# Kernel tuning notes

Measured on AMD Instinct MI355X. Metric: run time of the kernel, lower is better.

Reference implementation:

```python
import jax, jax.numpy as jnp
import numpy as np

N = 100000   # nodes
E = 1600000  # edges (avg degree 16)
D = 32       # feature dim

def setup_inputs() -> dict:
    key = jax.random.key(0)
    k1, k2, k3, k4 = jax.random.split(key, 4)
    feat = jax.random.normal(k1, (N, D), dtype=jnp.float32)
    e_feat = jax.random.normal(k2, (E, 1), dtype=jnp.float32)
    src = jax.random.randint(k3, (E,), 0, N)
    dst = jax.random.randint(k4, (E,), 0, N)
    return {"feat": feat, "e_feat": e_feat, "src": src, "dst": dst}

def reference(feat, e_feat, src, dst):
    n = feat.shape[0]
    ones = jnp.ones(src.shape[0], dtype=feat.dtype)
    # degrees computed on the full graph (before self-loop removal), as in DGL code
    out_deg = jax.ops.segment_sum(ones, src, num_segments=n)
    in_deg = jax.ops.segment_sum(ones, dst, num_segments=n)
    src_norm = jnp.power(jnp.clip(out_deg, 1.0, None), -0.5)[:, None]  # [N,1]
    dst_norm = jnp.power(jnp.clip(in_deg, 1.0, None), -0.5)[:, None]   # [N,1]
    # remove_self_loop: mask out self-loop edges in the aggregation only
    mask = (src != dst).astype(feat.dtype)[:, None]                    # [E,1]
    # u_mul_e: gather normalized src features, multiply by edge weight
    msg = (feat * src_norm)[src] * (e_feat * mask)                     # [E,D]
    agg = jax.ops.segment_sum(msg, dst, num_segments=n)                # [N,D]
    out = feat - agg * dst_norm
    return jnp.sum(jnp.abs(out), axis=1)                               # [N]
```

## Files before the change

kernel.cpp:

```cpp
#include <hip/hip_runtime.h>

#define D 32
#define RANGE 128
#define RMAX 800
#define JC 512
#define SCAN_CHUNK 4096
#define CAP 2560

__global__ void count_kernel(const int* __restrict__ src, const int* __restrict__ dst,
                             int* __restrict__ cnt, int E, int R, int chunk) {
    __shared__ int cd[RMAX];
    __shared__ int cs[RMAX];
    int j = blockIdx.x;
    for (int i = threadIdx.x; i < R; i += blockDim.x) { cd[i] = 0; cs[i] = 0; }
    __syncthreads();
    int e0 = j * chunk, e1 = min(E, e0 + chunk);
    for (int e = e0 + threadIdx.x; e < e1; e += blockDim.x) {
        atomicAdd(&cd[dst[e] >> 7], 1);
        atomicAdd(&cs[src[e] >> 7], 1);
    }
    __syncthreads();
    for (int i = threadIdx.x; i < R; i += blockDim.x) {
        cnt[(size_t)i * JC + j]       = cd[i];
        cnt[(size_t)(R + i) * JC + j] = cs[i];
    }
}

__global__ void scan_part(const int* __restrict__ deg, int* __restrict__ offsets,
                          int* __restrict__ blockSums, int n) {
    __shared__ int lds[256];
    int t = threadIdx.x;
    int base = blockIdx.x * SCAN_CHUNK + t * 16;
    int v[16];
    int tsum = 0;
#pragma unroll
    for (int i = 0; i < 16; i++) {
        int idx = base + i;
        int x = (idx < n) ? deg[idx] : 0;
        v[i] = tsum;
        tsum += x;
    }
    lds[t] = tsum;
    __syncthreads();
    for (int off = 1; off < 256; off <<= 1) {
        int val = (t >= off) ? lds[t - off] : 0;
        __syncthreads();
        lds[t] += val;
        __syncthreads();
    }
    int texcl = (t == 0) ? 0 : lds[t - 1];
    if (t == 255) blockSums[blockIdx.x] = lds[255];
#pragma unroll
    for (int i = 0; i < 16; i++) {
        int idx = base + i;
        if (idx < n) offsets[idx] = texcl + v[i];
    }
}

__global__ void scan_top(int* __restrict__ blockSums, int nb) {
    __shared__ int lds[256];
    int t = threadIdx.x;
    lds[t] = (t < nb) ? blockSums[t] : 0;
    __syncthreads();
    for (int off = 1; off < 256; off <<= 1) {
        int val = (t >= off) ? lds[t - off] : 0;
        __syncthreads();
        lds[t] += val;
        __syncthreads();
    }
    if (t < nb) blockSums[t] = (t == 0) ? 0 : lds[t - 1];
}

__global__ void scan_add(int* __restrict__ offsets, const int* __restrict__ blockSums, int n) {
    int i = blockIdx.x * blockDim.x + threadIdx.x;
    if (i < n) offsets[i] += blockSums[i / SCAN_CHUNK];
}

__global__ void reorder_kernel(const int* __restrict__ src, const int* __restrict__ dst,
                               const float* __restrict__ ef, const int* __restrict__ offs,
                               unsigned int* __restrict__ recsS_m, uint2* __restrict__ recs,
                               int E, int R, int chunk) {
    __shared__ int curD[RMAX];
    __shared__ int curS[RMAX];
    int j = blockIdx.x;
    for (int i = threadIdx.x; i < R; i += blockDim.x) {
        curD[i] = offs[(size_t)i * JC + j];
        curS[i] = offs[(size_t)(R + i) * JC + j];
    }
    __syncthreads();
    int e0 = j * chunk, e1 = min(E, e0 + chunk);
    for (int e = e0 + threadIdx.x; e < e1; e += blockDim.x) {
        int s = src[e], d = dst[e];
        int ps = atomicAdd(&curS[s >> 7], 1);
        recsS_m[ps] = (unsigned)s;
        float w = (s == d) ? 0.0f : ef[e];
        int pd = atomicAdd(&curD[d >> 7], 1);
        recs[pd] = make_uint2((unsigned)s | ((unsigned)(d & (RANGE - 1)) << 17),
                              __float_as_uint(w));
    }
}

__device__ __forceinline__ unsigned short f2bf(float x) {
    unsigned u = __float_as_uint(x);
    u += 0x7FFFu + ((u >> 16) & 1u);
    return (unsigned short)(u >> 16);
}

__global__ void srcnorm_convert(const unsigned int* __restrict__ recsS_m,
                                const int* __restrict__ offs, const float* __restrict__ feat,
                                unsigned short* __restrict__ featb, int E, int n, int R) {
    __shared__ int cnt[RANGE];
    int r = blockIdx.x;
    int base = r * RANGE;
    int lim = min(n - base, RANGE);
    for (int i = threadIdx.x; i < RANGE; i += blockDim.x) cnt[i] = 0;
    __syncthreads();
    int start = offs[(size_t)(R + r) * JC];
    int end = (r + 1 < R) ? offs[(size_t)(R + r + 1) * JC] : 2 * E;
    for (int i = start + threadIdx.x; i < end; i += blockDim.x)
        atomicAdd(&cnt[recsS_m[i] - base], 1);
    __syncthreads();
    int total4 = lim * 8;
    for (int i = threadIdx.x; i < total4; i += blockDim.x) {
        int row = i >> 3;
        float sn = rsqrtf((float)max(cnt[row], 1));
        float4 f = ((const float4*)(feat + (size_t)(base + row) * D))[i & 7];
        ushort4 u;
        u.x = f2bf(f.x * sn); u.y = f2bf(f.y * sn);
        u.z = f2bf(f.z * sn); u.w = f2bf(f.w * sn);
        ((ushort4*)(featb + (size_t)(base + row) * D))[i & 7] = u;
    }
}

__global__ __launch_bounds__(512) void gather_kernel(
        const float* __restrict__ feat, const unsigned short* __restrict__ featb,
        const uint2* __restrict__ recs, const int* __restrict__ offs,
        float* __restrict__ out, int E, int n, int R) {
    __shared__ uint2 srec[CAP];
    __shared__ int indeg[RANGE];
    __shared__ int pre[RANGE + 1];
    __shared__ int cur[RANGE];
    int r = blockIdx.x;
    int base = r * RANGE;
    int lim = min(n - base, RANGE);
    int start = offs[(size_t)r * JC];
    int end = (r + 1 < R) ? offs[(size_t)(r + 1) * JC] : E;
    int capEnd = min(end, start + CAP);
    for (int i = threadIdx.x; i < RANGE; i += blockDim.x) indeg[i] = 0;
    __syncthreads();
    for (int i = start + threadIdx.x; i < capEnd; i += blockDim.x)
        atomicAdd(&indeg[(recs[i].x >> 17) & 0x1FFu], 1);
    __syncthreads();
    if (threadIdx.x < RANGE) pre[threadIdx.x + 1] = indeg[threadIdx.x];
    if (threadIdx.x == 0) pre[0] = 0;
    __syncthreads();
    for (int off = 1; off < RANGE; off <<= 1) {
        int v = 0;
        if (threadIdx.x < RANGE) {
            int idx = threadIdx.x + 1;
            if (idx > off) v = pre[idx - off];
        }
        __syncthreads();
        if (threadIdx.x < RANGE) pre[threadIdx.x + 1] += v;
        __syncthreads();
    }
    if (threadIdx.x < RANGE) cur[threadIdx.x] = pre[threadIdx.x];
    __syncthreads();
    for (int i = start + threadIdx.x; i < capEnd; i += blockDim.x) {
        uint2 rec = recs[i];
        int dl = (rec.x >> 17) & 0x1FFu;
        int pos = atomicAdd(&cur[dl], 1);
        srec[pos] = make_uint2(rec.x & 0x1FFFFu, rec.y);
    }
    __syncthreads();
    int node = threadIdx.x >> 2;
    int c = threadIdx.x & 3;
    if (node >= lim) return;
    int p0i = pre[node];
    int cnt = pre[node + 1] - p0i;
    float a0 = 0.f, a1 = 0.f, a2 = 0.f, a3 = 0.f, a4 = 0.f, a5 = 0.f, a6 = 0.f, a7 = 0.f;
    int i = 0;
    for (; i + 2 <= cnt; i += 2) {
        uint2 q0 = srec[p0i + i];
        uint2 q1 = srec[p0i + i + 1];
        uint4 b0 = ((const uint4*)(featb + (size_t)q0.x * D))[c];
        uint4 b1 = ((const uint4*)(featb + (size_t)q1.x * D))[c];
        float w0 = __uint_as_float(q0.y);
        float w1 = __uint_as_float(q1.y);
        a0 += __uint_as_float(b0.x << 16) * w0 + __uint_as_float(b1.x << 16) * w1;
        a1 += __uint_as_float(b0.x & 0xFFFF0000u) * w0 + __uint_as_float(b1.x & 0xFFFF0000u) * w1;
        a2 += __uint_as_float(b0.y << 16) * w0 + __uint_as_float(b1.y << 16) * w1;
        a3 += __uint_as_float(b0.y & 0xFFFF0000u) * w0 + __uint_as_float(b1.y & 0xFFFF0000u) * w1;
        a4 += __uint_as_float(b0.z << 16) * w0 + __uint_as_float(b1.z << 16) * w1;
        a5 += __uint_as_float(b0.z & 0xFFFF0000u) * w0 + __uint_as_float(b1.z & 0xFFFF0000u) * w1;
        a6 += __uint_as_float(b0.w << 16) * w0 + __uint_as_float(b1.w << 16) * w1;
        a7 += __uint_as_float(b0.w & 0xFFFF0000u) * w0 + __uint_as_float(b1.w & 0xFFFF0000u) * w1;
    }
    if (i < cnt) {
        uint2 q = srec[p0i + i];
        uint4 b = ((const uint4*)(featb + (size_t)q.x * D))[c];
        float w = __uint_as_float(q.y);
        a0 += __uint_as_float(b.x << 16) * w;
        a1 += __uint_as_float(b.x & 0xFFFF0000u) * w;
        a2 += __uint_as_float(b.y << 16) * w;
        a3 += __uint_as_float(b.y & 0xFFFF0000u) * w;
        a4 += __uint_as_float(b.z << 16) * w;
        a5 += __uint_as_float(b.z & 0xFFFF0000u) * w;
        a6 += __uint_as_float(b.w << 16) * w;
        a7 += __uint_as_float(b.w & 0xFFFF0000u) * w;
    }
    if (end - start > CAP) {
        for (int k = start + CAP; k < end; k++) {
            uint2 rec = recs[k];
            int dl = (rec.x >> 17) & 0x1FFu;
            if (dl == node) {
                cnt++;
                uint4 b = ((const uint4*)(featb + (size_t)(rec.x & 0x1FFFFu) * D))[c];
                float w = __uint_as_float(rec.y);
                a0 += __uint_as_float(b.x << 16) * w;
                a1 += __uint_as_float(b.x & 0xFFFF0000u) * w;
                a2 += __uint_as_float(b.y << 16) * w;
                a3 += __uint_as_float(b.y & 0xFFFF0000u) * w;
                a4 += __uint_as_float(b.z << 16) * w;
                a5 += __uint_as_float(b.z & 0xFFFF0000u) * w;
                a6 += __uint_as_float(b.w << 16) * w;
                a7 += __uint_as_float(b.w & 0xFFFF0000u) * w;
            }
        }
    }
    float dn = rsqrtf((float)max(cnt, 1));
    const float4* fr = (const float4*)(feat + (size_t)(base + node) * D);
    float4 fA = fr[c * 2];
    float4 fB = fr[c * 2 + 1];
    float v = fabsf(fA.x - a0 * dn) + fabsf(fA.y - a1 * dn) +
              fabsf(fA.z - a2 * dn) + fabsf(fA.w - a3 * dn) +
              fabsf(fB.x - a4 * dn) + fabsf(fB.y - a5 * dn) +
              fabsf(fB.z - a6 * dn) + fabsf(fB.w - a7 * dn);
    v += __shfl_xor(v, 1, 4);
    v += __shfl_xor(v, 2, 4);
    if (c == 0) out[base + node] = v;
}

extern "C" void kernel_launch(void* const* d_in, const int* in_sizes, int n_in,
                              void* d_out, int out_size, void* d_ws, size_t ws_size,
                              hipStream_t stream) {
    const float* feat   = (const float*)d_in[0];
    const float* e_feat = (const float*)d_in[1];
    const int*   src    = (const int*)d_in[2];
    const int*   dst    = (const int*)d_in[3];
    const int E = in_sizes[2];
    const int n = in_sizes[0] / D;
    float* out = (float*)d_out;

    const int R = (n + RANGE - 1) / RANGE;
    const int chunk = (E + JC - 1) / JC;
    const int total = 2 * R * JC;

    char* p = (char*)d_ws;
    int* cnt       = (int*)p;   p += ((size_t)total * 4 + 15) & ~(size_t)15;
    int* offs      = (int*)p;   p += ((size_t)total * 4 + 15) & ~(size_t)15;
    int* blockSums = (int*)p;   p += 256 * 4;
    uint2* recs    = (uint2*)p; p += ((size_t)E * 8 + 15) & ~(size_t)15;
    unsigned int* recsS = (unsigned int*)p; p += ((size_t)E * 4 + 15) & ~(size_t)15;
    unsigned short* featb = (unsigned short*)p;
    unsigned int* recsS_m = recsS - (size_t)E;

    count_kernel<<<JC, 256, 0, stream>>>(src, dst, cnt, E, R, chunk);

    int nb = (total + SCAN_CHUNK - 1) / SCAN_CHUNK;
    scan_part<<<nb, 256, 0, stream>>>(cnt, offs, blockSums, total);
    scan_top<<<1, 256, 0, stream>>>(blockSums, nb);
    scan_add<<<(total + 255) / 256, 256, 0, stream>>>(offs, blockSums, total);

    reorder_kernel<<<JC, 256, 0, stream>>>(src, dst, e_feat, offs, recsS_m, recs, E, R, chunk);

    srcnorm_convert<<<R, 256, 0, stream>>>(recsS_m, offs, feat, featb, E, n, R);

    gather_kernel<<<R, 512, 0, stream>>>(feat, featb, recs, offs, out, E, n, R);
}
```

Measured before the change: 172.4 us.

## Replace global scan bucketing with per-chunk local sort and segmented gather

The separate count, three-stage global scan and scatter reorder kernels are merged into one kernel. It counts, scans and bucket-sorts each edge chunk in shared memory, then writes its records contiguously along with per-bucket (start,count) metadata. The srcnorm and gather kernels then read 512 small segments per bucket through that metadata instead of one globally contiguous range. This removes three kernel launches and the scattered global writes. In exchange the later stages make many short, uncoalesced segment reads, and there is a much slower fallback path when a bucket overflows the shared-memory capacity.

```diff
diff --git a/kernel.cpp b/kernel.cpp
--- a/kernel.cpp
+++ b/kernel.cpp
@@ -4,99 +4,74 @@
 #define RANGE 128
 #define RMAX 800
 #define JC 512
-#define SCAN_CHUNK 4096
+#define CHUNKMAX 3200
 #define CAP 2560
 
-__global__ void count_kernel(const int* __restrict__ src, const int* __restrict__ dst,
-                             int* __restrict__ cnt, int E, int R, int chunk) {
-    __shared__ int cd[RMAX];
-    __shared__ int cs[RMAX];
-    int j = blockIdx.x;
-    for (int i = threadIdx.x; i < R; i += blockDim.x) { cd[i] = 0; cs[i] = 0; }
-    __syncthreads();
-    int e0 = j * chunk, e1 = min(E, e0 + chunk);
-    for (int e = e0 + threadIdx.x; e < e1; e += blockDim.x) {
-        atomicAdd(&cd[dst[e] >> 7], 1);
-        atomicAdd(&cs[src[e] >> 7], 1);
-    }
-    __syncthreads();
-    for (int i = threadIdx.x; i < R; i += blockDim.x) {
-        cnt[(size_t)i * JC + j]       = cd[i];
-        cnt[(size_t)(R + i) * JC + j] = cs[i];
-    }
-}
-
-__global__ void scan_part(const int* __restrict__ deg, int* __restrict__ offsets,
-                          int* __restrict__ blockSums, int n) {
-    __shared__ int lds[256];
-    int t = threadIdx.x;
-    int base = blockIdx.x * SCAN_CHUNK + t * 16;
-    int v[16];
-    int tsum = 0;
-#pragma unroll
-    for (int i = 0; i < 16; i++) {
-        int idx = base + i;
-        int x = (idx < n) ? deg[idx] : 0;
-        v[i] = tsum;
-        tsum += x;
-    }
-    lds[t] = tsum;
-    __syncthreads();
-    for (int off = 1; off < 256; off <<= 1) {
-        int val = (t >= off) ? lds[t - off] : 0;
-        __syncthreads();
-        lds[t] += val;
-        __syncthreads();
-    }
-    int texcl = (t == 0) ? 0 : lds[t - 1];
-    if (t == 255) blockSums[blockIdx.x] = lds[255];
-#pragma unroll
-    for (int i = 0; i < 16; i++) {
-        int idx = base + i;
-        if (idx < n) offsets[idx] = texcl + v[i];
-    }
-}
-
-__global__ void scan_top(int* __restrict__ blockSums, int nb) {
-    __shared__ int lds[256];
-    int t = threadIdx.x;
-    lds[t] = (t < nb) ? blockSums[t] : 0;
-    __syncthreads();
-    for (int off = 1; off < 256; off <<= 1) {
-        int val = (t >= off) ? lds[t - off] : 0;
-        __syncthreads();
-        lds[t] += val;
-        __syncthreads();
-    }
-    if (t < nb) blockSums[t] = (t == 0) ? 0 : lds[t - 1];
-}
-
-__global__ void scan_add(int* __restrict__ offsets, const int* __restrict__ blockSums, int n) {
-    int i = blockIdx.x * blockDim.x + threadIdx.x;
-    if (i < n) offsets[i] += blockSums[i / SCAN_CHUNK];
-}
-
-__global__ void reorder_kernel(const int* __restrict__ src, const int* __restrict__ dst,
-                               const float* __restrict__ ef, const int* __restrict__ offs,
-                               unsigned int* __restrict__ recsS_m, uint2* __restrict__ recs,
-                               int E, int R, int chunk) {
-    __shared__ int curD[RMAX];
-    __shared__ int curS[RMAX];
-    int j = blockIdx.x;
-    for (int i = threadIdx.x; i < R; i += blockDim.x) {
-        curD[i] = offs[(size_t)i * JC + j];
-        curS[i] = offs[(size_t)(R + i) * JC + j];
-    }
-    __syncthreads();
-    int e0 = j * chunk, e1 = min(E, e0 + chunk);
-    for (int e = e0 + threadIdx.x; e < e1; e += blockDim.x) {
+__global__ __launch_bounds__(512) void sort_chunks(
+        const int* __restrict__ src, const int* __restrict__ dst,
+        const float* __restrict__ ef,
+        uint2* __restrict__ recs, unsigned* __restrict__ recsS,
+        unsigned* __restrict__ metaD, unsigned* __restrict__ metaS,
+        int E, int R, int chunk) {
+    __shared__ uint2 sd[CHUNKMAX];
+    __shared__ unsigned ss_[CHUNKMAX];
+    __shared__ int cd[RMAX], cs[RMAX];
+    __shared__ int curD[RMAX], curS[RMAX];
+    int j = blockIdx.x, t = threadIdx.x;
+    int e0 = j * chunk, e1 = min(E, e0 + chunk), cntE = e1 - e0;
+    for (int i = t; i < RMAX; i += 512) { cd[i] = 0; cs[i] = 0; }
+    __syncthreads();
+    for (int e = e0 + 2 * t; e < e1; e += 1024) {
+        if (e + 1 < e1) {
+            int2 s2 = *(const int2*)(src + e);
+            int2 d2 = *(const int2*)(dst + e);
+            atomicAdd(&cd[d2.x >> 7], 1);
+            atomicAdd(&cd[d2.y >> 7], 1);
+            atomicAdd(&cs[s2.x >> 7], 1);
+            atomicAdd(&cs[s2.y >> 7], 1);
+        } else {
+            atomicAdd(&cd[dst[e] >> 7], 1);
+            atomicAdd(&cs[src[e] >> 7], 1);
+        }
+    }
+    __syncthreads();
+    {
+        int i1 = t + 512;
+        curD[t] = cd[t]; curS[t] = cs[t];
+        if (i1 < RMAX) { curD[i1] = cd[i1]; curS[i1] = cs[i1]; }
+        __syncthreads();
+        for (int off = 1; off < RMAX; off <<= 1) {
+            int vD0 = (t >= off) ? curD[t - off] : 0;
+            int vS0 = (t >= off) ? curS[t - off] : 0;
+            int vD1 = 0, vS1 = 0;
+            if (i1 < RMAX && i1 >= off) { vD1 = curD[i1 - off]; vS1 = curS[i1 - off]; }
+            __syncthreads();
+            curD[t] += vD0; curS[t] += vS0;
+            if (i1 < RMAX) { curD[i1] += vD1; curS[i1] += vS1; }
+            __syncthreads();
+        }
+        curD[t] -= cd[t]; curS[t] -= cs[t];
+        if (i1 < RMAX) { curD[i1] -= cd[i1]; curS[i1] -= cs[i1]; }
+        __syncthreads();
+    }
+    for (int e = e0 + t; e < e1; e += 512) {
         int s = src[e], d = dst[e];
+        float w = (s == d) ? 0.0f : ef[e];
+        int pos = atomicAdd(&curD[d >> 7], 1);
+        sd[pos] = make_uint2((unsigned)s | ((unsigned)(d & (RANGE - 1)) << 17),
+                             __float_as_uint(w));
         int ps = atomicAdd(&curS[s >> 7], 1);
-        recsS_m[ps] = (unsigned)s;
-        float w = (s == d) ? 0.0f : ef[e];
-        int pd = atomicAdd(&curD[d >> 7], 1);
-        recs[pd] = make_uint2((unsigned)s | ((unsigned)(d & (RANGE - 1)) << 17),
-                              __float_as_uint(w));
+        ss_[ps] = (unsigned)s;
+    }
+    __syncthreads();
+    size_t baseE = (size_t)j * chunk;
+    for (int i = t; i < cntE; i += 512) {
+        recs[baseE + i] = sd[i];
+        recsS[baseE + i] = ss_[i];
+    }
+    for (int i = t; i < R; i += 512) {
+        metaD[(size_t)j * R + i] = ((unsigned)(curD[i] - cd[i]) << 16) | (unsigned)cd[i];
+        metaS[(size_t)j * R + i] = ((unsigned)(curS[i] - cs[i]) << 16) | (unsigned)cs[i];
     }
 }
 
@@ -106,22 +81,22 @@
     return (unsigned short)(u >> 16);
 }
 
-__global__ void srcnorm_convert(const unsigned int* __restrict__ recsS_m,
-                                const int* __restrict__ offs, const float* __restrict__ feat,
-                                unsigned short* __restrict__ featb, int E, int n, int R) {
+__global__ __launch_bounds__(512) void srcnorm_convert(
+        const unsigned* __restrict__ recsS, const unsigned* __restrict__ metaS,
+        const float* __restrict__ feat, unsigned short* __restrict__ featb,
+        int n, int R, int chunk) {
     __shared__ int cnt[RANGE];
-    int r = blockIdx.x;
-    int base = r * RANGE;
-    int lim = min(n - base, RANGE);
-    for (int i = threadIdx.x; i < RANGE; i += blockDim.x) cnt[i] = 0;
-    __syncthreads();
-    int start = offs[(size_t)(R + r) * JC];
-    int end = (r + 1 < R) ? offs[(size_t)(R + r + 1) * JC] : 2 * E;
-    for (int i = start + threadIdx.x; i < end; i += blockDim.x)
-        atomicAdd(&cnt[recsS_m[i] - base], 1);
+    int r = blockIdx.x, t = threadIdx.x;
+    int base = r * RANGE, lim = min(n - base, RANGE);
+    if (t < RANGE) cnt[t] = 0;
+    __syncthreads();
+    unsigned m = metaS[(size_t)t * R + r];
+    int st = m >> 16, c = m & 0xFFFFu;
+    const unsigned* p = recsS + (size_t)t * chunk + st;
+    for (int k = 0; k < c; k++) atomicAdd(&cnt[p[k] - (unsigned)base], 1);
     __syncthreads();
     int total4 = lim * 8;
-    for (int i = threadIdx.x; i < total4; i += blockDim.x) {
+    for (int i = t; i < total4; i += 512) {
         int row = i >> 3;
         float sn = rsqrtf((float)max(cnt[row], 1));
         float4 f = ((const float4*)(feat + (size_t)(base + row) * D))[i & 7];
@@ -134,111 +109,133 @@
 
 __global__ __launch_bounds__(512) void gather_kernel(
         const float* __restrict__ feat, const unsigned short* __restrict__ featb,
-        const uint2* __restrict__ recs, const int* __restrict__ offs,
-        float* __restrict__ out, int E, int n, int R) {
+        const uint2* __restrict__ recs, const unsigned* __restrict__ metaD,
+        float* __restrict__ out, int n, int R, int chunk) {
+    __shared__ uint2 raw[CAP];
     __shared__ uint2 srec[CAP];
+    __shared__ int segpre[JC + 1];
     __shared__ int indeg[RANGE];
     __shared__ int pre[RANGE + 1];
     __shared__ int cur[RANGE];
-    int r = blockIdx.x;
-    int base = r * RANGE;
-    int lim = min(n - base, RANGE);
-    int start = offs[(size_t)r * JC];
-    int end = (r + 1 < R) ? offs[(size_t)(r + 1) * JC] : E;
-    int capEnd = min(end, start + CAP);
-    for (int i = threadIdx.x; i < RANGE; i += blockDim.x) indeg[i] = 0;
-    __syncthreads();
-    for (int i = start + threadIdx.x; i < capEnd; i += blockDim.x)
-        atomicAdd(&indeg[(recs[i].x >> 17) & 0x1FFu], 1);
-    __syncthreads();
-    if (threadIdx.x < RANGE) pre[threadIdx.x + 1] = indeg[threadIdx.x];
-    if (threadIdx.x == 0) pre[0] = 0;
+    int r = blockIdx.x, t = threadIdx.x;
+    int base = r * RANGE, lim = min(n - base, RANGE);
+    unsigned m = metaD[(size_t)t * R + r];
+    int st = m >> 16, c = m & 0xFFFFu;
+    segpre[t + 1] = c;
+    if (t == 0) segpre[0] = 0;
+    if (t < RANGE) indeg[t] = 0;
+    __syncthreads();
+    for (int off = 1; off < JC; off <<= 1) {
+        int v = (t + 1 > off) ? segpre[t + 1 - off] : 0;
+        __syncthreads();
+        segpre[t + 1] += v;
+        __syncthreads();
+    }
+    int total = segpre[JC];
+    bool ovf = total > CAP;
+    const uint2* p = recs + (size_t)t * chunk + st;
+    if (!ovf) {
+        int dp = segpre[t];
+        for (int k = 0; k < c; k++) {
+            uint2 rec = p[k];
+            raw[dp + k] = rec;
+            atomicAdd(&indeg[rec.x >> 17], 1);
+        }
+    } else {
+        for (int k = 0; k < c; k++) atomicAdd(&indeg[p[k].x >> 17], 1);
+    }
+    __syncthreads();
+    if (t < RANGE) pre[t + 1] = indeg[t];
+    if (t == 0) pre[0] = 0;
     __syncthreads();
     for (int off = 1; off < RANGE; off <<= 1) {
         int v = 0;
-        if (threadIdx.x < RANGE) {
-            int idx = threadIdx.x + 1;
-            if (idx > off) v = pre[idx - off];
-        }
-        __syncthreads();
-        if (threadIdx.x < RANGE) pre[threadIdx.x + 1] += v;
-        __syncthreads();
-    }
-    if (threadIdx.x < RANGE) cur[threadIdx.x] = pre[threadIdx.x];
-    __syncthreads();
-    for (int i = start + threadIdx.x; i < capEnd; i += blockDim.x) {
-        uint2 rec = recs[i];
-        int dl = (rec.x >> 17) & 0x1FFu;
-        int pos = atomicAdd(&cur[dl], 1);
-        srec[pos] = make_uint2(rec.x & 0x1FFFFu, rec.y);
-    }
-    __syncthreads();
-    int node = threadIdx.x >> 2;
-    int c = threadIdx.x & 3;
+        if (t < RANGE) { int idx = t + 1; if (idx > off) v = pre[idx - off]; }
+        __syncthreads();
+        if (t < RANGE) pre[t + 1] += v;
+        __syncthreads();
+    }
+    if (t < RANGE) cur[t] = pre[t];
+    __syncthreads();
+    if (!ovf) {
+        for (int i = t; i < total; i += 512) {
+            uint2 rec = raw[i];
+            int dl = rec.x >> 17;
+            int pos = atomicAdd(&cur[dl], 1);
+            srec[pos] = make_uint2(rec.x & 0x1FFFFu, rec.y);
+        }
+    }
+    __syncthreads();
+    int node = t >> 2;
+    int cch = t & 3;
     if (node >= lim) return;
     int p0i = pre[node];
     int cnt = pre[node + 1] - p0i;
     float a0 = 0.f, a1 = 0.f, a2 = 0.f, a3 = 0.f, a4 = 0.f, a5 = 0.f, a6 = 0.f, a7 = 0.f;
-    int i = 0;
-    for (; i + 2 <= cnt; i += 2) {
-        uint2 q0 = srec[p0i + i];
-        uint2 q1 = srec[p0i + i + 1];
-        uint4 b0 = ((const uint4*)(featb + (size_t)q0.x * D))[c];
-        uint4 b1 = ((const uint4*)(featb + (size_t)q1.x * D))[c];
-        float w0 = __uint_as_float(q0.y);
-        float w1 = __uint_as_float(q1.y);
-        a0 += __uint_as_float(b0.x << 16) * w0 + __uint_as_float(b1.x << 16) * w1;
-        a1 += __uint_as_float(b0.x & 0xFFFF0000u) * w0 + __uint_as_float(b1.x & 0xFFFF0000u) * w1;
-        a2 += __uint_as_float(b0.y << 16) * w0 + __uint_as_float(b1.y << 16) * w1;
-        a3 += __uint_as_float(b0.y & 0xFFFF0000u) * w0 + __uint_as_float(b1.y & 0xFFFF0000u) * w1;
-        a4 += __uint_as_float(b0.z << 16) * w0 + __uint_as_float(b1.z << 16) * w1;
-        a5 += __uint_as_float(b0.z & 0xFFFF0000u) * w0 + __uint_as_float(b1.z & 0xFFFF0000u) * w1;
-        a6 += __uint_as_float(b0.w << 16) * w0 + __uint_as_float(b1.w << 16) * w1;
-        a7 += __uint_as_float(b0.w & 0xFFFF0000u) * w0 + __uint_as_float(b1.w & 0xFFFF0000u) * w1;
-    }
-    if (i < cnt) {
-        uint2 q = srec[p0i + i];
-        uint4 b = ((const uint4*)(featb + (size_t)q.x * D))[c];
-        float w = __uint_as_float(q.y);
-        a0 += __uint_as_float(b.x << 16) * w;
-        a1 += __uint_as_float(b.x & 0xFFFF0000u) * w;
-        a2 += __uint_as_float(b.y << 16) * w;
-        a3 += __uint_as_float(b.y & 0xFFFF0000u) * w;
-        a4 += __uint_as_float(b.z << 16) * w;
-        a5 += __uint_as_float(b.z & 0xFFFF0000u) * w;
-        a6 += __uint_as_float(b.w << 16) * w;
-        a7 += __uint_as_float(b.w & 0xFFFF0000u) * w;
-    }
-    if (end - start > CAP) {
-        for (int k = start + CAP; k < end; k++) {
-            uint2 rec = recs[k];
-            int dl = (rec.x >> 17) & 0x1FFu;
-            if (dl == node) {
-                cnt++;
-                uint4 b = ((const uint4*)(featb + (size_t)(rec.x & 0x1FFFFu) * D))[c];
-                float w = __uint_as_float(rec.y);
-                a0 += __uint_as_float(b.x << 16) * w;
-                a1 += __uint_as_float(b.x & 0xFFFF0000u) * w;
-                a2 += __uint_as_float(b.y << 16) * w;
-                a3 += __uint_as_float(b.y & 0xFFFF0000u) * w;
-                a4 += __uint_as_float(b.z << 16) * w;
-                a5 += __uint_as_float(b.z & 0xFFFF0000u) * w;
-                a6 += __uint_as_float(b.w << 16) * w;
-                a7 += __uint_as_float(b.w & 0xFFFF0000u) * w;
+    if (!ovf) {
+        int i = 0;
+        for (; i + 2 <= cnt; i += 2) {
+            uint2 q0 = srec[p0i + i];
+            uint2 q1 = srec[p0i + i + 1];
+            uint4 b0 = ((const uint4*)(featb + (size_t)q0.x * D))[cch];
+            uint4 b1 = ((const uint4*)(featb + (size_t)q1.x * D))[cch];
+            float w0 = __uint_as_float(q0.y);
+            float w1 = __uint_as_float(q1.y);
+            a0 += __uint_as_float(b0.x << 16) * w0 + __uint_as_float(b1.x << 16) * w1;
+            a1 += __uint_as_float(b0.x & 0xFFFF0000u) * w0 + __uint_as_float(b1.x & 0xFFFF0000u) * w1;
+            a2 += __uint_as_float(b0.y << 16) * w0 + __uint_as_float(b1.y << 16) * w1;
+            a3 += __uint_as_float(b0.y & 0xFFFF0000u) * w0 + __uint_as_float(b1.y & 0xFFFF0000u) * w1;
+            a4 += __uint_as_float(b0.z << 16) * w0 + __uint_as_float(b1.z << 16) * w1;
+            a5 += __uint_as_float(b0.z & 0xFFFF0000u) * w0 + __uint_as_float(b1.z & 0xFFFF0000u) * w1;
+            a6 += __uint_as_float(b0.w << 16) * w0 + __uint_as_float(b1.w << 16) * w1;
+            a7 += __uint_as_float(b0.w & 0xFFFF0000u) * w0 + __uint_as_float(b1.w & 0xFFFF0000u) * w1;
+        }
+        if (i < cnt) {
+            uint2 q = srec[p0i + i];
+            uint4 b = ((const uint4*)(featb + (size_t)q.x * D))[cch];
+            float w = __uint_as_float(q.y);
+            a0 += __uint_as_float(b.x << 16) * w;
+            a1 += __uint_as_float(b.x & 0xFFFF0000u) * w;
+            a2 += __uint_as_float(b.y << 16) * w;
+            a3 += __uint_as_float(b.y & 0xFFFF0000u) * w;
+            a4 += __uint_as_float(b.z << 16) * w;
+            a5 += __uint_as_float(b.z & 0xFFFF0000u) * w;
+            a6 += __uint_as_float(b.w << 16) * w;
+            a7 += __uint_as_float(b.w & 0xFFFF0000u) * w;
+        }
+    } else {
+        for (int j = 0; j < JC; j++) {
+            unsigned mm = metaD[(size_t)j * R + r];
+            const uint2* pp = recs + (size_t)j * chunk + (mm >> 16);
+            int cc = mm & 0xFFFFu;
+            for (int k = 0; k < cc; k++) {
+                uint2 rec = pp[k];
+                if ((int)(rec.x >> 17) == node) {
+                    uint4 b = ((const uint4*)(featb + (size_t)(rec.x & 0x1FFFFu) * D))[cch];
+                    float w = __uint_as_float(rec.y);
+                    a0 += __uint_as_float(b.x << 16) * w;
+                    a1 += __uint_as_float(b.x & 0xFFFF0000u) * w;
+                    a2 += __uint_as_float(b.y << 16) * w;
+                    a3 += __uint_as_float(b.y & 0xFFFF0000u) * w;
+                    a4 += __uint_as_float(b.z << 16) * w;
+                    a5 += __uint_as_float(b.z & 0xFFFF0000u) * w;
+                    a6 += __uint_as_float(b.w << 16) * w;
+                    a7 += __uint_as_float(b.w & 0xFFFF0000u) * w;
+                }
             }
         }
     }
     float dn = rsqrtf((float)max(cnt, 1));
     const float4* fr = (const float4*)(feat + (size_t)(base + node) * D);
-    float4 fA = fr[c * 2];
-    float4 fB = fr[c * 2 + 1];
+    float4 fA = fr[cch * 2];
+    float4 fB = fr[cch * 2 + 1];
     float v = fabsf(fA.x - a0 * dn) + fabsf(fA.y - a1 * dn) +
               fabsf(fA.z - a2 * dn) + fabsf(fA.w - a3 * dn) +
               fabsf(fB.x - a4 * dn) + fabsf(fB.y - a5 * dn) +
               fabsf(fB.z - a6 * dn) + fabsf(fB.w - a7 * dn);
     v += __shfl_xor(v, 1, 4);
     v += __shfl_xor(v, 2, 4);
-    if (c == 0) out[base + node] = v;
+    if (cch == 0) out[base + node] = v;
 }
 
 extern "C" void kernel_launch(void* const* d_in, const int* in_sizes, int n_in,
@@ -253,28 +250,19 @@
     float* out = (float*)d_out;
 
     const int R = (n + RANGE - 1) / RANGE;
-    const int chunk = (E + JC - 1) / JC;
-    const int total = 2 * R * JC;
+    const int chunk = (((E + JC - 1) / JC) + 1) & ~1;
 
     char* p = (char*)d_ws;
-    int* cnt       = (int*)p;   p += ((size_t)total * 4 + 15) & ~(size_t)15;
-    int* offs      = (int*)p;   p += ((size_t)total * 4 + 15) & ~(size_t)15;
-    int* blockSums = (int*)p;   p += 256 * 4;
-    uint2* recs    = (uint2*)p; p += ((size_t)E * 8 + 15) & ~(size_t)15;
-    unsigned int* recsS = (unsigned int*)p; p += ((size_t)E * 4 + 15) & ~(size_t)15;
+    uint2* recs    = (uint2*)p;    p += ((size_t)JC * chunk * 8 + 15) & ~(size_t)15;
+    unsigned* recsS = (unsigned*)p; p += ((size_t)JC * chunk * 4 + 15) & ~(size_t)15;
+    unsigned* metaD = (unsigned*)p; p += ((size_t)JC * R * 4 + 15) & ~(size_t)15;
+    unsigned* metaS = (unsigned*)p; p += ((size_t)JC * R * 4 + 15) & ~(size_t)15;
     unsigned short* featb = (unsigned short*)p;
-    unsigned int* recsS_m = recsS - (size_t)E;
-
-    count_kernel<<<JC, 256, 0, stream>>>(src, dst, cnt, E, R, chunk);
-
-    int nb = (total + SCAN_CHUNK - 1) / SCAN_CHUNK;
-    scan_part<<<nb, 256, 0, stream>>>(cnt, offs, blockSums, total);
-    scan_top<<<1, 256, 0, stream>>>(blockSums, nb);
-    scan_add<<<(total + 255) / 256, 256, 0, stream>>>(offs, blockSums, total);
-
-    reorder_kernel<<<JC, 256, 0, stream>>>(src, dst, e_feat, offs, recsS_m, recs, E, R, chunk);
-
-    srcnorm_convert<<<R, 256, 0, stream>>>(recsS_m, offs, feat, featb, E, n, R);
-
-    gather_kernel<<<R, 512, 0, stream>>>(feat, featb, recs, offs, out, E, n, R);
-}
+
+    sort_chunks<<<JC, 512, 0, stream>>>(src, dst, e_feat, recs, recsS, metaD, metaS,
+                                        E, R, chunk);
+
+    srcnorm_convert<<<R, 512, 0, stream>>>(recsS, metaS, feat, featb, n, R, chunk);
+
+    gather_kernel<<<R, 512, 0, stream>>>(feat, featb, recs, metaD, out, n, R, chunk);
+}
```

Measured after the change: 150.4 us. 1.15x faster.
